# Kernel optimization log

Hardware: AMD Instinct MI355X
Metric: run time of the kernel (lower is better)

Reference implementation:

```python
import jax, jax.numpy as jnp
import numpy as np

B, S, D, H = 2, 2048, 2048, 16
DH = D // H  # 128
EPS = 1e-6


def _rms_norm(x, w):
    # RMSNorm over last dim with learnable scale
    var = jnp.mean(jnp.square(x), axis=-1, keepdims=True)
    return x * jax.lax.rsqrt(var + EPS) * w


def _apply_rope(x, angles):
    # x: [B, S, H, DH]; angles: [S, DH//2]; interleaved pair rotation
    xs = x.reshape(*x.shape[:-1], DH // 2, 2)
    x0, x1 = xs[..., 0], xs[..., 1]
    cos = jnp.cos(angles)[None, :, None, :]  # [1,S,1,DH/2]
    sin = jnp.sin(angles)[None, :, None, :]
    r0 = x0 * cos - x1 * sin
    r1 = x0 * sin + x1 * cos
    return jnp.stack([r0, r1], axis=-1).reshape(x.shape)


def setup_inputs() -> dict:
    key = jax.random.key(0)
    ks = jax.random.split(key, 4)
    x = jax.random.normal(ks[0], (B, S, D), dtype=jnp.float32)
    # standard RoPE angle table: pos * inv_freq
    inv_freq = 1.0 / (10000.0 ** (jnp.arange(0, DH, 2, dtype=jnp.float32) / DH))
    pos = jnp.arange(S, dtype=jnp.float32)
    rp_freqs = pos[:, None] * inv_freq[None, :]  # [S, DH/2]
    Win = jax.random.normal(ks[1], (3 * D, D), dtype=jnp.float32) * (D ** -0.5)
    b_in = jnp.zeros((3 * D,), dtype=jnp.float32)
    Wout = jax.random.normal(ks[2], (D, D), dtype=jnp.float32) * (D ** -0.5)
    b_out = jnp.zeros((D,), dtype=jnp.float32)
    qk_w = jnp.ones((DH,), dtype=jnp.float32)
    out_w = jnp.ones((D,), dtype=jnp.float32)
    return {"x": x, "rp_freqs": rp_freqs, "Win": Win, "b_in": b_in,
            "Wout": Wout, "b_out": b_out, "qk_w": qk_w, "out_w": out_w}


def reference(x, rp_freqs, Win, b_in, Wout, b_out, qk_w, out_w):
    b, s, d = x.shape
    qkv = jnp.einsum('bsd,ed->bse', x, Win) + b_in  # [B,S,3D]
    qkv = qkv.reshape(b, s, 3, H, DH)
    q, k, v = qkv[:, :, 0], qkv[:, :, 1], qkv[:, :, 2]  # each [B,S,H,DH]
    q = _apply_rope(q, rp_freqs)
    k = _apply_rope(k, rp_freqs)
    q = _rms_norm(q, qk_w)
    k = _rms_norm(k, qk_w)
    # causal SDPA, scale = 1/sqrt(DH) (default)
    a = jax.nn.dot_product_attention(q, k, v, is_causal=True)  # [B,S,H,DH]
    a = a.reshape(b, s, d)
    a = _rms_norm(a, out_w)
    return jnp.einsum('bsd,ed->bse', a, Wout) + b_out
```

## Files before the change

### kernel.cpp

```cpp
#include <hip/hip_runtime.h>
#include <cstdint>
#include <cstddef>

#define Bq  2
#define Sq  2048
#define Dq  2048
#define Hq  16
#define DHq 128
#define E3q 6144

typedef __attribute__((ext_vector_type(8))) short s16x8;
typedef __attribute__((ext_vector_type(4))) float f32x4;

__device__ __forceinline__ unsigned short f2bf(float f){
  union { float f; unsigned u; } v; v.f = f;
  unsigned r = v.u + 0x7FFFu + ((v.u >> 16) & 1u);
  return (unsigned short)(r >> 16);
}
__device__ __forceinline__ float bf2f(unsigned short b){
  union { unsigned u; float f; } v; v.u = ((unsigned)b) << 16;
  return v.f;
}
__device__ __forceinline__ unsigned cvtpk_bf16(float lo, float hi){
  unsigned r;
  asm("v_cvt_pk_bf16_f32 %0, %1, %2" : "=v"(r) : "v"(lo), "v"(hi));
  return r;
}

__device__ __forceinline__ void gload_lds16(const void* g, void* l){
  __builtin_amdgcn_global_load_lds(
      (const __attribute__((address_space(1))) void*)g,
      (__attribute__((address_space(3))) void*)l, 16, 0, 0);
}

__global__ __launch_bounds__(256) void k_convert3(const float* __restrict__ x,
                                                  const float* __restrict__ win,
                                                  const float* __restrict__ wout,
                                                  const float* __restrict__ out_w,
                                                  const float* __restrict__ rp,
                                                  unsigned short* __restrict__ xb,
                                                  unsigned short* __restrict__ wb,
                                                  unsigned short* __restrict__ woutb,
                                                  float2* __restrict__ rpcs){
  const int NX = (Bq*Sq*Dq)/4;
  const int NW = (E3q*Dq)/4;
  const int NO = (Dq*Dq)/4;
  const int NR = (Sq*64)/4;
  const int total = NX + NW + NO + NR;
  int stride = gridDim.x * blockDim.x;
  for (int i = blockIdx.x*blockDim.x + threadIdx.x; i < total; i += stride){
    if (i < NX + NW){
      const float* src; unsigned short* dst; int j;
      if (i < NX){ src = x; dst = xb; j = i; }
      else { src = win; dst = wb; j = i - NX; }
      float4 v = reinterpret_cast<const float4*>(src)[j];
      ushort4 o;
      o.x = f2bf(v.x); o.y = f2bf(v.y); o.z = f2bf(v.z); o.w = f2bf(v.w);
      reinterpret_cast<ushort4*>(dst)[j] = o;
    } else if (i < NX + NW + NO){
      int j = i - NX - NW;
      float4 v = reinterpret_cast<const float4*>(wout)[j];
      float4 w = reinterpret_cast<const float4*>(out_w)[j & 511];
      ushort4 o;
      o.x = f2bf(v.x*w.x); o.y = f2bf(v.y*w.y); o.z = f2bf(v.z*w.z); o.w = f2bf(v.w*w.w);
      reinterpret_cast<ushort4*>(woutb)[j] = o;
    } else {
      int j = i - NX - NW - NO;
      float4 a = reinterpret_cast<const float4*>(rp)[j];
      float sn0,cs0,sn1,cs1,sn2,cs2,sn3,cs3;
      sincosf(a.x,&sn0,&cs0); sincosf(a.y,&sn1,&cs1);
      sincosf(a.z,&sn2,&cs2); sincosf(a.w,&sn3,&cs3);
      float4 p0 = make_float4(cs0,sn0,cs1,sn1);
      float4 p1 = make_float4(cs2,sn2,cs3,sn3);
      reinterpret_cast<float4*>(rpcs)[j*2  ] = p0;
      reinterpret_cast<float4*>(rpcs)[j*2+1] = p1;
    }
  }
}

__global__ __launch_bounds__(512, 1) void k_gemm1f(const unsigned short* __restrict__ A,
                                                   const unsigned short* __restrict__ Bt,
                                                   const float* __restrict__ bias,
                                                   const float2* __restrict__ rpcs,
                                                   const float* __restrict__ qk_w,
                                                   unsigned short* __restrict__ Qp,
                                                   unsigned short* __restrict__ Kp,
                                                   unsigned short* __restrict__ Vt){
  const int K = 2048, NI = 16;
  const int bid = blockIdx.x;
  const int xcd = bid & 7, u = bid >> 3;
  const int m0 = (xcd*4 + (u & 3)) * 128;
  const int n0 = (u >> 2) * 256;

  const int tid = threadIdx.x;
  const int lane = tid & 63, w = tid >> 6, g = lane >> 4, c = lane & 15;
  const int wm = w >> 2, wn = w & 3;

  __shared__ __align__(16) unsigned short L[49152];

  const int srow = tid >> 2, spc = tid & 3;
  const int ssw = (spc ^ ((srow >> 1) & 3)) << 3;
  const unsigned short* aSrc  = A  + (size_t)(m0 + srow      )*K + ssw;
  const unsigned short* bSrc0 = Bt + (size_t)(n0 + srow      )*K + ssw;
  const unsigned short* bSrc1 = Bt + (size_t)(n0 + srow + 128)*K + ssw;

  auto stA = [&](int t, int h){
    gload_lds16(aSrc + t*64 + h*32, &L[((t&1)*2 + h)*4096 + tid*8]);
  };
  auto stB = [&](int t, int h, int uu){
    const unsigned short* s = (uu==0) ? bSrc0 : bSrc1;
    gload_lds16(s + t*64 + h*32, &L[16384 + ((t&1)*2 + h)*8192 + uu*4096 + tid*8]);
  };

  int aoff[4], boff[4];
#pragma unroll
  for (int mf=0; mf<4; ++mf){
    int row = wm*64 + mf*16 + c;
    aoff[mf] = row*32 + ((g ^ ((row>>1)&3)) << 3);
  }
#pragma unroll
  for (int nf=0; nf<4; ++nf){
    int row = wn*64 + nf*16 + c;
    boff[nf] = row*32 + ((g ^ ((row>>1)&3)) << 3);
  }

  f32x4 acc[4][4];
#pragma unroll
  for (int i=0;i<4;i++)
#pragma unroll
    for (int j=0;j<4;j++)
#pragma unroll
      for (int r=0;r<4;r++) acc[i][j][r] = 0.f;

  auto RDA = [&](int b, int h, s16x8* af){
    const int ab = (b*2 + h)*4096;
#pragma unroll
    for (int mf=0; mf<4; ++mf) af[mf] = *(const s16x8*)&L[ab + aoff[mf]];
  };
  auto RDB = [&](int b, int h, int nh, s16x8* bf){
    const int bb = 16384 + (b*2 + h)*8192;
#pragma unroll
    for (int j=0; j<2; ++j) bf[j] = *(const s16x8*)&L[bb + boff[nh*2 + j]];
  };
  auto MM = [&](s16x8* af, s16x8* bf, int nh){
    __builtin_amdgcn_s_setprio(1);
#pragma unroll
    for (int mf=0; mf<4; ++mf)
#pragma unroll
      for (int j=0; j<2; ++j)
        acc[mf][nh*2+j] = __builtin_amdgcn_mfma_f32_16x16x32_bf16(af[mf], bf[j], acc[mf][nh*2+j], 0,0,0);
    __builtin_amdgcn_s_setprio(0);
  };
  auto BAR = [&](){
    __builtin_amdgcn_sched_barrier(0);
    __builtin_amdgcn_s_barrier();
    __builtin_amdgcn_sched_barrier(0);
  };

  stA(0,0); stB(0,0,0); stB(0,0,1);
  stA(0,1); stB(0,1,0); stB(0,1,1);
  stA(1,0); stB(1,0,0); stB(1,0,1);
  asm volatile("s_waitcnt vmcnt(3)" ::: "memory");
  __builtin_amdgcn_s_barrier();

  for (int i=0; i<NI; ++i){
    const int T0 = 2*i, T1 = 2*i + 1;
    const bool st = (i < NI-1);
    s16x8 af[4], bf[2];
    RDA(0,0,af); RDB(0,0,0,bf);
    stA(T1,1); stB(T1,1,0);
    BAR(); MM(af,bf,0); BAR();
    RDB(0,0,1,bf);
    stB(T1,1,1);
    BAR(); MM(af,bf,1); BAR();
    RDA(0,1,af); RDB(0,1,0,bf);
    if (st){ stA(T0+2,0); stB(T0+2,0,0); }
    BAR(); MM(af,bf,0); BAR();
    RDB(0,1,1,bf);
    if (st){ stB(T0+2,0,1); }
    __builtin_amdgcn_sched_barrier(0);
    if (st) asm volatile("s_waitcnt vmcnt(3)" ::: "memory");
    else    asm volatile("s_waitcnt vmcnt(0)" ::: "memory");
    BAR(); MM(af,bf,1); BAR();
    RDA(1,0,af); RDB(1,0,0,bf);
    if (st){ stA(T0+2,1); stB(T0+2,1,0); }
    BAR(); MM(af,bf,0); BAR();
    RDB(1,0,1,bf);
    if (st){ stB(T0+2,1,1); }
    BAR(); MM(af,bf,1); BAR();
    RDA(1,1,af); RDB(1,1,0,bf);
    if (st){ stA(T1+2,0); stB(T1+2,0,0); }
    BAR(); MM(af,bf,0); BAR();
    RDB(1,1,1,bf);
    if (st){ stB(T1+2,0,1); }
    __builtin_amdgcn_sched_barrier(0);
    if (st) asm volatile("s_waitcnt vmcnt(3)" ::: "memory");
    else    asm volatile("s_waitcnt vmcnt(0)" ::: "memory");
    BAR(); MM(af,bf,1); BAR();
  }

  const int btype = (n0 < 2048) ? 0 : (n0 < 4096) ? 1 : 2;
  const int b  = m0 >> 11;
  const int sb = m0 & 2047;
  const int h0 = (n0 & 2047) >> 7;
  const int LTS = 264;
  const float QSCALE = 0.08838834764831845f * 1.4426950408889634f;

#pragma unroll
  for (int nf=0; nf<4; ++nf){
    const float bv = bias[n0 + wn*64 + nf*16 + c];
#pragma unroll
    for (int mf=0; mf<4; ++mf)
#pragma unroll
      for (int r=0; r<4; ++r) acc[mf][nf][r] += bv;
  }

  __syncthreads();

  if (btype < 2){
    float s2[4][4];
#pragma unroll
    for (int mf=0;mf<4;mf++)
#pragma unroll
      for (int r=0;r<4;r++){
        float s = 0.f;
#pragma unroll
        for (int nf=0;nf<4;nf++){ float v = acc[mf][nf][r]; s += v*v; }
        s2[mf][r] = s;
      }
#pragma unroll
    for (int m=1;m<16;m<<=1)
#pragma unroll
      for (int mf=0;mf<4;mf++)
#pragma unroll
        for (int r=0;r<4;r++) s2[mf][r] += __shfl_xor(s2[mf][r], m);
    float* Ssum = (float*)&L[0];
    if (c==0 && (wn&1)==0){
#pragma unroll
      for (int mf=0;mf<4;mf++)
#pragma unroll
        for (int r=0;r<4;r++)
          Ssum[(wm*64+mf*16+g*4+r)*2 + (wn>>1)] = s2[mf][r];
    }
    __syncthreads();
    if (c==0 && (wn&1)==1){
#pragma unroll
      for (int mf=0;mf<4;mf++)
#pragma unroll
        for (int r=0;r<4;r++)
          Ssum[(wm*64+mf*16+g*4+r)*2 + (wn>>1)] += s2[mf][r];
    }
    __syncthreads();
    float rsc[4][4];
#pragma unroll
    for (int mf=0;mf<4;mf++)
#pragma unroll
      for (int r=0;r<4;r++)
        rsc[mf][r] = rsqrtf(Ssum[(wm*64+mf*16+g*4+r)*2 + (wn>>1)]*(1.f/128.f) + 1e-6f);
    __syncthreads();

    const float qmul = (btype==0) ? QSCALE : 1.f;
    float wq[4];
    int pp[4];
#pragma unroll
    for (int nf=0;nf<4;nf++){
      wq[nf] = qk_w[(wn*64+nf*16+c)&127];
      pp[nf] = ((wn*64+nf*16+c)&127) >> 1;
    }

#pragma unroll
    for (int mf=0;mf<4;mf++)
#pragma unroll
      for (int r=0;r<4;r++){
        const int rowl = wm*64+mf*16+g*4+r;
        const int s = sb + rowl;
        const float sc = rsc[mf][r] * qmul;
#pragma unroll
        for (int nf=0;nf<4;nf++){
          float2 t = rpcs[s*64 + pp[nf]];
          float v  = acc[mf][nf][r];
          float pv = __shfl_xor(v, 1);
          float rot = ((c&1)==0) ? (v*t.x - pv*t.y) : (pv*t.y + v*t.x);
          L[rowl*LTS + wn*64+nf*16+c] = f2bf(rot * sc * wq[nf]);
        }
      }
    __syncthreads();
    {
      const int rw = tid >> 2, hd = (tid>>1)&1, hf = tid&1;
      const int bh = b*Hq + h0 + hd;
      unsigned short* dst = ((btype==0) ? Qp : Kp)
                          + ((size_t)bh*Sq + sb + rw)*DHq + hf*64;
      const unsigned short* srcl = &L[rw*LTS + hd*128 + hf*64];
#pragma unroll
      for (int i2=0;i2<8;i2++)
        *(s16x8*)&dst[i2*8] = *(const s16x8*)&srcl[i2*8];
    }
  } else {
#pragma unroll
    for (int mf=0;mf<4;mf++)
#pragma unroll
      for (int r=0;r<4;r++){
        const int rowl = wm*64+mf*16+g*4+r;
#pragma unroll
        for (int nf=0;nf<4;nf++)
          L[rowl*LTS + wn*64+nf*16+c] = f2bf(acc[mf][nf][r]);
      }
    __syncthreads();
    {
      const int dh2 = tid >> 1, hfr = (tid & 1) * 64;
      const int hd = dh2 >> 7, dh = dh2 & 127;
      const int bh = b*Hq + h0 + hd;
      unsigned short buf[64];
#pragma unroll
      for (int i2=0;i2<64;i2++) buf[i2] = L[(hfr+i2)*LTS + dh2];
      unsigned short* dst = Vt + ((size_t)bh*DHq + dh)*Sq + sb + hfr;
#pragma unroll
      for (int i2=0;i2<8;i2++)
        *(s16x8*)&dst[i2*8] = *(const s16x8*)&buf[i2*8];
    }
  }
}

__global__ __launch_bounds__(512, 1) void k_gemm2_8ph(const unsigned short* __restrict__ A,
                                                      const unsigned short* __restrict__ Bt,
                                                      const float* __restrict__ bias,
                                                      const float* __restrict__ ssqp,
                                                      float* __restrict__ C){
  const int K = 2048, N = 2048, NI = 16;
  const int bid = blockIdx.x;
  const int xcd = bid & 7, u = bid >> 3;
  const int m0 = (xcd*4 + (u & 3)) * 128;
  const int n0 = (u >> 2) * 256;

  const int tid = threadIdx.x;
  const int lane = tid & 63, w = tid >> 6, g = lane >> 4, c = lane & 15;
  const int wm = w >> 2, wn = w & 3;

  __shared__ __align__(16) unsigned short L[49152];

  const int srow = tid >> 2, spc = tid & 3;
  const int ssw = (spc ^ ((srow >> 1) & 3)) << 3;
  const unsigned short* aSrc  = A  + (size_t)(m0 + srow      )*K + ssw;
  const unsigned short* bSrc0 = Bt + (size_t)(n0 + srow      )*K + ssw;
  const unsigned short* bSrc1 = Bt + (size_t)(n0 + srow + 128)*K + ssw;

  auto stA = [&](int t, int h){
    gload_lds16(aSrc + t*64 + h*32, &L[((t&1)*2 + h)*4096 + tid*8]);
  };
  auto stB = [&](int t, int h, int uu){
    const unsigned short* s = (uu==0) ? bSrc0 : bSrc1;
    gload_lds16(s + t*64 + h*32, &L[16384 + ((t&1)*2 + h)*8192 + uu*4096 + tid*8]);
  };

  int aoff[4], boff[4];
#pragma unroll
  for (int mf=0; mf<4; ++mf){
    int row = wm*64 + mf*16 + c;
    aoff[mf] = row*32 + ((g ^ ((row>>1)&3)) << 3);
  }
#pragma unroll
  for (int nf=0; nf<4; ++nf){
    int row = wn*64 + nf*16 + c;
    boff[nf] = row*32 + ((g ^ ((row>>1)&3)) << 3);
  }

  f32x4 acc[4][4];
#pragma unroll
  for (int i=0;i<4;i++)
#pragma unroll
    for (int j=0;j<4;j++)
#pragma unroll
      for (int r=0;r<4;r++) acc[i][j][r] = 0.f;

  auto RDA = [&](int b, int h, s16x8* af){
    const int ab = (b*2 + h)*4096;
#pragma unroll
    for (int mf=0; mf<4; ++mf) af[mf] = *(const s16x8*)&L[ab + aoff[mf]];
  };
  auto RDB = [&](int b, int h, int nh, s16x8* bf){
    const int bb = 16384 + (b*2 + h)*8192;
#pragma unroll
    for (int j=0; j<2; ++j) bf[j] = *(const s16x8*)&L[bb + boff[nh*2 + j]];
  };
  auto MM = [&](s16x8* af, s16x8* bf, int nh){
    __builtin_amdgcn_s_setprio(1);
#pragma unroll
    for (int mf=0; mf<4; ++mf)
#pragma unroll
      for (int j=0; j<2; ++j)
        acc[mf][nh*2+j] = __builtin_amdgcn_mfma_f32_16x16x32_bf16(af[mf], bf[j], acc[mf][nh*2+j], 0,0,0);
    __builtin_amdgcn_s_setprio(0);
  };
  auto BAR = [&](){
    __builtin_amdgcn_sched_barrier(0);
    __builtin_amdgcn_s_barrier();
    __builtin_amdgcn_sched_barrier(0);
  };

  stA(0,0); stB(0,0,0); stB(0,0,1);
  stA(0,1); stB(0,1,0); stB(0,1,1);
  stA(1,0); stB(1,0,0); stB(1,0,1);
  asm volatile("s_waitcnt vmcnt(3)" ::: "memory");
  __builtin_amdgcn_s_barrier();

  for (int i=0; i<NI; ++i){
    const int T0 = 2*i, T1 = 2*i + 1;
    const bool st = (i < NI-1);
    s16x8 af[4], bf[2];
    RDA(0,0,af); RDB(0,0,0,bf);
    stA(T1,1); stB(T1,1,0);
    BAR(); MM(af,bf,0); BAR();
    RDB(0,0,1,bf);
    stB(T1,1,1);
    BAR(); MM(af,bf,1); BAR();
    RDA(0,1,af); RDB(0,1,0,bf);
    if (st){ stA(T0+2,0); stB(T0+2,0,0); }
    BAR(); MM(af,bf,0); BAR();
    RDB(0,1,1,bf);
    if (st){ stB(T0+2,0,1); }
    __builtin_amdgcn_sched_barrier(0);
    if (st) asm volatile("s_waitcnt vmcnt(3)" ::: "memory");
    else    asm volatile("s_waitcnt vmcnt(0)" ::: "memory");
    BAR(); MM(af,bf,1); BAR();
    RDA(1,0,af); RDB(1,0,0,bf);
    if (st){ stA(T0+2,1); stB(T0+2,1,0); }
    BAR(); MM(af,bf,0); BAR();
    RDB(1,0,1,bf);
    if (st){ stB(T0+2,1,1); }
    BAR(); MM(af,bf,1); BAR();
    RDA(1,1,af); RDB(1,1,0,bf);
    if (st){ stA(T1+2,0); stB(T1+2,0,0); }
    BAR(); MM(af,bf,0); BAR();
    RDB(1,1,1,bf);
    if (st){ stB(T1+2,0,1); }
    __builtin_amdgcn_sched_barrier(0);
    if (st) asm volatile("s_waitcnt vmcnt(3)" ::: "memory");
    else    asm volatile("s_waitcnt vmcnt(0)" ::: "memory");
    BAR(); MM(af,bf,1); BAR();
  }

  __syncthreads();
  float* SS = (float*)&L[0];
  if (tid < 128){
    const float* p = ssqp + (size_t)(m0 + tid)*16;
    float s = 0.f;
#pragma unroll
    for (int h=0; h<16; ++h) s += p[h];
    SS[tid] = rsqrtf(s*(1.f/2048.f) + 1e-6f);
  }
  __syncthreads();

#pragma unroll
  for (int nf=0; nf<4; ++nf){
    const int col = n0 + wn*64 + nf*16 + c;
    const float bv = bias[col];
#pragma unroll
    for (int mf=0; mf<4; ++mf){
      const int rowl = wm*64 + mf*16 + g*4;
#pragma unroll
      for (int r=0; r<4; ++r)
        C[(size_t)(m0+rowl+r)*N + col] = acc[mf][nf][r]*SS[rowl+r] + bv;
    }
  }
}

__global__ __launch_bounds__(256, 2) void k_attn(const unsigned short* __restrict__ Qp,
                                                 const unsigned short* __restrict__ Kp,
                                                 const unsigned short* __restrict__ Vt,
                                                 unsigned short* __restrict__ Ar,
                                                 float* __restrict__ ssqp){
  const int L = blockIdx.x;
  const int xcdL = L & 7, j = L >> 3;
  const int bh = xcdL*4 + ((j & 31) >> 3);
  const int qtile = (j < 32) ? (8 + (j & 7)) : (7 - (j & 7));
  const int b = bh >> 4, h = bh & 15;
  const int tid = threadIdx.x;
  const int w = tid >> 6, lane = tid & 63, g = lane >> 4, c = lane & 15;
  const int r0w = qtile*128 + w*32;

  const unsigned short* Qh = Qp + (size_t)bh * Sq * DHq;
  const unsigned short* Kh = Kp + (size_t)bh * Sq * DHq;
  const unsigned short* Vh = Vt + (size_t)bh * DHq * Sq;

  __shared__ __align__(16) unsigned short Ks[2][64*128];
  __shared__ __align__(16) unsigned short Vs[2][128*64];
  __shared__ __align__(16) unsigned short Pl[4][32*64];
  unsigned short* Pw = &Pl[w][0];

  s16x8 qf[2][4];
#pragma unroll
  for (int mi=0;mi<2;mi++)
#pragma unroll
    for (int kc=0;kc<4;kc++)
      qf[mi][kc] = *(const s16x8*)&Qh[(size_t)(r0w + mi*16 + c)*DHq + kc*32 + g*8];

  f32x4 acc[2][8];
#pragma unroll
  for (int mi=0;mi<2;mi++)
#pragma unroll
    for (int dt=0;dt<8;dt++)
#pragma unroll
      for (int r=0;r<4;r++) acc[mi][dt][r] = 0.f;
  float m_r[2] = { -INFINITY, -INFINITY };
  float l_p[2] = { 0.f, 0.f };

  const int nsteps = 2*qtile + 2;

  auto stage = [&](int j0s, int bufi){
#pragma unroll
    for (int i=0;i<4;i++){
      int pk = tid + i*256;
      int row = pk>>4, pcc = pk&15;
      gload_lds16(&Kh[(size_t)(j0s+row)*DHq + ((pcc^(row&7))<<3)], &Ks[bufi][pk*8]);
    }
#pragma unroll
    for (int i=0;i<4;i++){
      int pk = tid + i*256;
      int row = pk>>3, pcc = pk&7;
      gload_lds16(&Vh[(size_t)row*Sq + j0s + ((pcc^(row&7))<<3)], &Vs[bufi][pk*8]);
    }
  };

  stage(0, 0);
  __syncthreads();

  for (int t=0; t<nsteps; ++t){
    const int j0 = t*64;
    if (t+1 < nsteps) stage((t+1)*64, (t+1)&1);

    if (j0 <= r0w + 31){
      const unsigned short* Kc = &Ks[t&1][0];
      const unsigned short* Vc = &Vs[t&1][0];

      f32x4 sv[2][4];
#pragma unroll
      for (int mi=0;mi<2;mi++)
#pragma unroll
        for (int js=0;js<4;js++)
#pragma unroll
          for (int r=0;r<4;r++) sv[mi][js][r] = 0.f;

      __builtin_amdgcn_s_setprio(1);
#pragma unroll
      for (int js=0;js<4;js++){
        s16x8 kf[4];
#pragma unroll
        for (int kc=0;kc<4;kc++)
          kf[kc] = *(const s16x8*)&Kc[(js*16 + c)*128 + (((kc*4+g)^(c&7))<<3)];
#pragma unroll
        for (int mi=0;mi<2;mi++)
#pragma unroll
          for (int kc=0;kc<4;kc++)
            sv[mi][js] = __builtin_amdgcn_mfma_f32_16x16x32_bf16(kf[kc], qf[mi][kc], sv[mi][js], 0,0,0);
      }
      __builtin_amdgcn_s_setprio(0);

      if (j0 + 63 > r0w){
#pragma unroll
        for (int mi=0;mi<2;mi++){
          const int q = r0w + mi*16 + c;
#pragma unroll
          for (int js=0;js<4;js++)
#pragma unroll
            for (int r=0;r<4;r++)
              if (j0 + js*16 + g*4 + r > q) sv[mi][js][r] = -INFINITY;
        }
      }

      float pmx[2];
#pragma unroll
      for (int mi=0;mi<2;mi++){
        float mx = fmaxf(fmaxf(sv[mi][0][0],sv[mi][0][1]), fmaxf(sv[mi][0][2],sv[mi][0][3]));
#pragma unroll
        for (int js=1;js<4;js++){
          float a = fmaxf(fmaxf(sv[mi][js][0],sv[mi][js][1]), fmaxf(sv[mi][js][2],sv[mi][js][3]));
          mx = fmaxf(mx, a);
        }
        mx = fmaxf(mx, __shfl_xor(mx, 16));
        mx = fmaxf(mx, __shfl_xor(mx, 32));
        pmx[mi] = mx;
      }
      int need = (pmx[0] > m_r[0] + 8.f) | (pmx[1] > m_r[1] + 8.f);
      if (__any(need)){
#pragma unroll
        for (int mi=0;mi<2;mi++){
          float mnew = fmaxf(m_r[mi], pmx[mi]);
          float corr = exp2f(m_r[mi] - mnew);
          l_p[mi] *= corr;
          m_r[mi] = mnew;
#pragma unroll
          for (int dt=0;dt<8;dt++)
#pragma unroll
            for (int r=0;r<4;r++) acc[mi][dt][r] *= corr;
        }
      }
#pragma unroll
      for (int mi=0;mi<2;mi++){
        const float mm = m_r[mi];
        const int rowoff = (mi*16 + c)*64;
#pragma unroll
        for (int js=0;js<4;js++){
          float e0 = exp2f(sv[mi][js][0] - mm);
          float e1 = exp2f(sv[mi][js][1] - mm);
          float e2 = exp2f(sv[mi][js][2] - mm);
          float e3 = exp2f(sv[mi][js][3] - mm);
          l_p[mi] += (e0+e1)+(e2+e3);
          uint2 pk2;
          pk2.x = cvtpk_bf16(e0, e1);
          pk2.y = cvtpk_bf16(e2, e3);
          const int kc8 = js*2 + (g>>1);
          *(uint2*)&Pw[rowoff + ((kc8 ^ (c&7))<<3) + (g&1)*4] = pk2;
        }
      }

      s16x8 pfr[2][2];
#pragma unroll
      for (int mi=0;mi<2;mi++)
#pragma unroll
        for (int kc=0;kc<2;kc++)
          pfr[mi][kc] = *(const s16x8*)&Pw[(mi*16 + c)*64 + (((kc*4+g)^(c&7))<<3)];
      __builtin_amdgcn_s_setprio(1);
#pragma unroll
      for (int dt=0; dt<8; dt++){
#pragma unroll
        for (int kc=0;kc<2;kc++){
          s16x8 vfr = *(const s16x8*)&Vc[(dt*16 + c)*64 + (((kc*4+g)^(c&7))<<3)];
#pragma unroll
          for (int mi=0;mi<2;mi++)
            acc[mi][dt] = __builtin_amdgcn_mfma_f32_16x16x32_bf16(vfr, pfr[mi][kc], acc[mi][dt], 0,0,0);
        }
      }
      __builtin_amdgcn_s_setprio(0);
    }
    __syncthreads();
  }

#pragma unroll
  for (int mi=0;mi<2;mi++){
    float l = l_p[mi];
    l += __shfl_xor(l, 16);
    l += __shfl_xor(l, 32);
    const float inv = 1.f / l;
    const int row = r0w + mi*16 + c;
    unsigned short* dst = &Ar[((size_t)(b*Sq + row))*Dq + h*DHq];
    float sq = 0.f;
#pragma unroll
    for (int dt=0; dt<8; dt++){
      float v0 = acc[mi][dt][0]*inv, v1 = acc[mi][dt][1]*inv;
      float v2 = acc[mi][dt][2]*inv, v3 = acc[mi][dt][3]*inv;
      sq += v0*v0 + v1*v1 + v2*v2 + v3*v3;
      uint2 o2;
      o2.x = cvtpk_bf16(v0, v1);
      o2.y = cvtpk_bf16(v2, v3);
      *(uint2*)&dst[dt*16 + g*4] = o2;
    }
    sq += __shfl_xor(sq, 16);
    sq += __shfl_xor(sq, 32);
    if (g == 0)
      ssqp[(size_t)(b*Sq + row)*16 + h] = sq;
  }
}

extern "C" void kernel_launch(void* const* d_in, const int* in_sizes, int n_in,
                              void* d_out, int out_size, void* d_ws, size_t ws_size,
                              hipStream_t stream){
  const float* x     = (const float*)d_in[0];
  const float* rp    = (const float*)d_in[1];
  const float* Win   = (const float*)d_in[2];
  const float* b_in  = (const float*)d_in[3];
  const float* Wout  = (const float*)d_in[4];
  const float* b_out = (const float*)d_in[5];
  const float* qk_w  = (const float*)d_in[6];
  const float* out_w = (const float*)d_in[7];
  float* outp = (float*)d_out;

  if (ws_size < (160ull<<20)) return;

  char* ws = (char*)d_ws;
  unsigned short* Xb    = (unsigned short*)(ws);
  unsigned short* Wb    = (unsigned short*)(ws + (16ull<<20));
  unsigned short* Woutb = (unsigned short*)(ws + (40ull<<20));
  float*          ssqp  = (float*)         (ws + (48ull<<20));
  float2*         rpcs  = (float2*)        (ws + (49ull<<20));
  unsigned short* Qp    = (unsigned short*)(ws + (96ull<<20));
  unsigned short* Kp    = (unsigned short*)(ws + (112ull<<20));
  unsigned short* Vt    = (unsigned short*)(ws + (128ull<<20));
  unsigned short* Ar    = (unsigned short*)(ws + (144ull<<20));

  k_convert3<<<2048, 256, 0, stream>>>(x, Win, Wout, out_w, rp, Xb, Wb, Woutb, rpcs);
  k_gemm1f<<<768, 512, 0, stream>>>(Xb, Wb, b_in, rpcs, qk_w, Qp, Kp, Vt);
  k_attn<<<512, 256, 0, stream>>>(Qp, Kp, Vt, Ar, ssqp);
  k_gemm2_8ph<<<256, 512, 0, stream>>>(Ar, Woutb, b_out, ssqp, outp);
}
```

Before: 262.0 us.

## Widen QKV GEMM tile to 128x384 so 512 blocks cover the grid once

The fused QKV projection kernel now computes 128x384 output tiles instead of 128x256, so the grid shrinks from 768 to 512 blocks. With one block per CU, that should avoid a partial second wave on the 256-CU device and raise A-tile reuse. A 384-wide tile can straddle head and Q/K/V boundaries, so the epilogue now tracks two heads per wave for the RMS sums and writes per column type. LDS use grows to 128KB and the accumulator registers grow by half, which may pressure occupancy and registers.

```diff
diff --git a/kernel.cpp b/kernel.cpp
--- a/kernel.cpp
+++ b/kernel.cpp
@@ -86,7 +86,275 @@
                                                    unsigned short* __restrict__ Qp,
                                                    unsigned short* __restrict__ Kp,
                                                    unsigned short* __restrict__ Vt){
-  const int K = 2048, NI = 16;
+  const int K = 2048;
+  const int bid = blockIdx.x;
+  const int xcd = bid & 7, u = bid >> 3;
+  const int m0 = (xcd*4 + (u & 3)) * 128;
+  const int n0 = (u >> 2) * 384;
+
+  const int tid = threadIdx.x;
+  const int lane = tid & 63, w = tid >> 6, g = lane >> 4, c = lane & 15;
+  const int wm = w >> 2, wn = w & 3;
+
+  __shared__ __align__(16) unsigned short L[65536];
+
+  const int srow = tid >> 2, spc = tid & 3;
+  const int ssw = (spc ^ ((srow >> 1) & 3)) << 3;
+  const unsigned short* aSrc  = A  + (size_t)(m0 + srow      )*K + ssw;
+  const unsigned short* bSrc0 = Bt + (size_t)(n0 + srow      )*K + ssw;
+  const unsigned short* bSrc1 = Bt + (size_t)(n0 + srow + 128)*K + ssw;
+  const unsigned short* bSrc2 = Bt + (size_t)(n0 + srow + 256)*K + ssw;
+
+  auto stA = [&](int t, int h){
+    gload_lds16(aSrc + t*64 + h*32, &L[((t&1)*2 + h)*4096 + tid*8]);
+  };
+  auto stB = [&](int t, int h, int uu){
+    const unsigned short* s = (uu==0) ? bSrc0 : (uu==1) ? bSrc1 : bSrc2;
+    gload_lds16(s + t*64 + h*32, &L[16384 + ((t&1)*2 + h)*12288 + uu*4096 + tid*8]);
+  };
+
+  int aoff[4], boff[6];
+#pragma unroll
+  for (int mf=0; mf<4; ++mf){
+    int row = wm*64 + mf*16 + c;
+    aoff[mf] = row*32 + ((g ^ ((row>>1)&3)) << 3);
+  }
+#pragma unroll
+  for (int nf=0; nf<6; ++nf){
+    int row = wn*96 + nf*16 + c;
+    boff[nf] = row*32 + ((g ^ ((row>>1)&3)) << 3);
+  }
+
+  f32x4 acc[4][6];
+#pragma unroll
+  for (int i=0;i<4;i++)
+#pragma unroll
+    for (int j=0;j<6;j++)
+#pragma unroll
+      for (int r=0;r<4;r++) acc[i][j][r] = 0.f;
+
+  auto RDA = [&](int b, int h, s16x8* af){
+    const int ab = (b*2 + h)*4096;
+#pragma unroll
+    for (int mf=0; mf<4; ++mf) af[mf] = *(const s16x8*)&L[ab + aoff[mf]];
+  };
+  auto RDB = [&](int b, int h, int nh, s16x8* bf){
+    const int bb = 16384 + (b*2 + h)*12288;
+#pragma unroll
+    for (int j=0; j<3; ++j) bf[j] = *(const s16x8*)&L[bb + boff[nh*3 + j]];
+  };
+  auto MM = [&](s16x8* af, s16x8* bf, int nh){
+    __builtin_amdgcn_s_setprio(1);
+#pragma unroll
+    for (int mf=0; mf<4; ++mf)
+#pragma unroll
+      for (int j=0; j<3; ++j)
+        acc[mf][nh*3+j] = __builtin_amdgcn_mfma_f32_16x16x32_bf16(af[mf], bf[j], acc[mf][nh*3+j], 0,0,0);
+    __builtin_amdgcn_s_setprio(0);
+  };
+  auto BAR = [&](){
+    __builtin_amdgcn_sched_barrier(0);
+    __builtin_amdgcn_s_barrier();
+    __builtin_amdgcn_sched_barrier(0);
+  };
+
+  stA(0,0); stB(0,0,0); stB(0,0,1); stB(0,0,2);
+  stA(0,1); stB(0,1,0); stB(0,1,1); stB(0,1,2);
+  stA(1,0); stB(1,0,0); stB(1,0,1); stB(1,0,2);
+  asm volatile("s_waitcnt vmcnt(4)" ::: "memory");
+  __builtin_amdgcn_s_barrier();
+
+  for (int i=0; i<16; ++i){
+    const int T0 = 2*i, T1 = 2*i + 1;
+    const bool st = (i < 15);
+    s16x8 af[4], bf[3];
+    RDA(0,0,af); RDB(0,0,0,bf);
+    stA(T1,1); stB(T1,1,0);
+    BAR(); MM(af,bf,0); BAR();
+    RDB(0,0,1,bf);
+    stB(T1,1,1); stB(T1,1,2);
+    BAR(); MM(af,bf,1); BAR();
+    RDA(0,1,af); RDB(0,1,0,bf);
+    if (st){ stA(T0+2,0); stB(T0+2,0,0); }
+    BAR(); MM(af,bf,0); BAR();
+    RDB(0,1,1,bf);
+    if (st){ stB(T0+2,0,1); stB(T0+2,0,2); }
+    __builtin_amdgcn_sched_barrier(0);
+    if (st) asm volatile("s_waitcnt vmcnt(4)" ::: "memory");
+    else    asm volatile("s_waitcnt vmcnt(0)" ::: "memory");
+    BAR(); MM(af,bf,1); BAR();
+    RDA(1,0,af); RDB(1,0,0,bf);
+    if (st){ stA(T0+2,1); stB(T0+2,1,0); }
+    BAR(); MM(af,bf,0); BAR();
+    RDB(1,0,1,bf);
+    if (st){ stB(T0+2,1,1); stB(T0+2,1,2); }
+    BAR(); MM(af,bf,1); BAR();
+    RDA(1,1,af); RDB(1,1,0,bf);
+    if (st){ stA(T1+2,0); stB(T1+2,0,0); }
+    BAR(); MM(af,bf,0); BAR();
+    RDB(1,1,1,bf);
+    if (st){ stB(T1+2,0,1); stB(T1+2,0,2); }
+    __builtin_amdgcn_sched_barrier(0);
+    if (st) asm volatile("s_waitcnt vmcnt(4)" ::: "memory");
+    else    asm volatile("s_waitcnt vmcnt(0)" ::: "memory");
+    BAR(); MM(af,bf,1); BAR();
+  }
+
+  const int b  = m0 >> 11;
+  const int sb = m0 & 2047;
+  const int LTS = 392;
+  const float QSCALE = 0.08838834764831845f * 1.4426950408889634f;
+  const int hdA = (wn*96) >> 7;
+
+#pragma unroll
+  for (int nf=0; nf<6; ++nf){
+    const float bv = bias[n0 + wn*96 + nf*16 + c];
+#pragma unroll
+    for (int mf=0; mf<4; ++mf)
+#pragma unroll
+      for (int r=0; r<4; ++r) acc[mf][nf][r] += bv;
+  }
+
+  __syncthreads();
+
+  float sA[4][4], sB[4][4];
+#pragma unroll
+  for (int mf=0;mf<4;mf++)
+#pragma unroll
+    for (int r=0;r<4;r++){ sA[mf][r] = 0.f; sB[mf][r] = 0.f; }
+#pragma unroll
+  for (int nf=0; nf<6; ++nf){
+    const int hd_nf = (wn*96 + nf*16) >> 7;
+    if (hd_nf == hdA){
+#pragma unroll
+      for (int mf=0;mf<4;mf++)
+#pragma unroll
+        for (int r=0;r<4;r++){ float v = acc[mf][nf][r]; sA[mf][r] += v*v; }
+    } else {
+#pragma unroll
+      for (int mf=0;mf<4;mf++)
+#pragma unroll
+        for (int r=0;r<4;r++){ float v = acc[mf][nf][r]; sB[mf][r] += v*v; }
+    }
+  }
+#pragma unroll
+  for (int m=1;m<16;m<<=1)
+#pragma unroll
+    for (int mf=0;mf<4;mf++)
+#pragma unroll
+      for (int r=0;r<4;r++){
+        sA[mf][r] += __shfl_xor(sA[mf][r], m);
+        sB[mf][r] += __shfl_xor(sB[mf][r], m);
+      }
+
+  float* SS = (float*)&L[50176];
+  if (c == 0){
+#pragma unroll
+    for (int mf=0;mf<4;mf++)
+#pragma unroll
+      for (int r=0;r<4;r++){
+        const int row = wm*64 + mf*16 + g*4 + r;
+        if (wn == 0) SS[row*3 + 0] = sA[mf][r];
+        else if (wn == 1) SS[row*3 + 1] = sB[mf][r];
+        else if (wn == 2) SS[row*3 + 2] = sB[mf][r];
+      }
+  }
+  __syncthreads();
+  if (c == 0){
+#pragma unroll
+    for (int mf=0;mf<4;mf++)
+#pragma unroll
+      for (int r=0;r<4;r++){
+        const int row = wm*64 + mf*16 + g*4 + r;
+        if (wn == 1) SS[row*3 + 0] += sA[mf][r];
+        else if (wn == 2) SS[row*3 + 1] += sA[mf][r];
+        else if (wn == 3) SS[row*3 + 2] += sA[mf][r];
+      }
+  }
+  __syncthreads();
+
+  const int hdB = (hdA < 2) ? hdA + 1 : 2;
+  float rA[4][4], rB[4][4];
+#pragma unroll
+  for (int mf=0;mf<4;mf++)
+#pragma unroll
+    for (int r=0;r<4;r++){
+      const int row = wm*64 + mf*16 + g*4 + r;
+      rA[mf][r] = rsqrtf(SS[row*3 + hdA]*(1.f/128.f) + 1e-6f);
+      rB[mf][r] = rsqrtf(SS[row*3 + hdB]*(1.f/128.f) + 1e-6f);
+    }
+  __syncthreads();
+
+  float wq[6]; int pp[6];
+#pragma unroll
+  for (int nf=0;nf<6;nf++){
+    const int cw = (wn*96 + nf*16 + c) & 127;
+    wq[nf] = qk_w[cw];
+    pp[nf] = cw >> 1;
+  }
+#pragma unroll
+  for (int nf=0; nf<6; ++nf){
+    const int colw = wn*96 + nf*16 + c;
+    const int bt = (n0 + colw) >> 11;
+    const int hd_nf = colw >> 7;
+    if (bt < 2){
+#pragma unroll
+      for (int mf=0;mf<4;mf++)
+#pragma unroll
+        for (int r=0;r<4;r++){
+          const int row = wm*64 + mf*16 + g*4 + r;
+          const float rs = (hd_nf == hdA) ? rA[mf][r] : rB[mf][r];
+          const float sc = rs * ((bt==0) ? QSCALE : 1.f);
+          float v  = acc[mf][nf][r];
+          float pv = __shfl_xor(v, 1);
+          float2 t = rpcs[(sb + row)*64 + pp[nf]];
+          float rot = ((c&1)==0) ? (v*t.x - pv*t.y) : (pv*t.y + v*t.x);
+          L[row*LTS + colw] = f2bf(rot * sc * wq[nf]);
+        }
+    } else {
+#pragma unroll
+      for (int mf=0;mf<4;mf++)
+#pragma unroll
+        for (int r=0;r<4;r++){
+          const int row = wm*64 + mf*16 + g*4 + r;
+          L[row*LTS + colw] = f2bf(acc[mf][nf][r]);
+        }
+    }
+  }
+  __syncthreads();
+
+#pragma unroll
+  for (int hd=0; hd<3; ++hd){
+    const int base = n0 + hd*128;
+    if (base < 4096){
+      const bool isQ = (base < 2048);
+      const int bh = b*Hq + ((base & 2047) >> 7);
+      const int rw = tid >> 2, part = tid & 3;
+      unsigned short* dst = (isQ ? Qp : Kp) + ((size_t)bh*Sq + sb + rw)*DHq + part*32;
+      const unsigned short* srcl = &L[rw*LTS + hd*128 + part*32];
+#pragma unroll
+      for (int i2=0;i2<4;i2++)
+        *(s16x8*)&dst[i2*8] = *(const s16x8*)&srcl[i2*8];
+    } else {
+      const int bh = b*Hq + ((base - 4096) >> 7);
+      const int dh = tid & 127, sg = tid >> 7;
+      unsigned short buf[32];
+#pragma unroll
+      for (int i2=0;i2<32;i2++) buf[i2] = L[(sg*32 + i2)*LTS + hd*128 + dh];
+      unsigned short* dst = Vt + ((size_t)bh*DHq + dh)*Sq + sb + sg*32;
+#pragma unroll
+      for (int i2=0;i2<4;i2++)
+        *(s16x8*)&dst[i2*8] = *(const s16x8*)&buf[i2*8];
+    }
+  }
+}
+
+__global__ __launch_bounds__(512, 1) void k_gemm2_8ph(const unsigned short* __restrict__ A,
+                                                      const unsigned short* __restrict__ Bt,
+                                                      const float* __restrict__ bias,
+                                                      const float* __restrict__ ssqp,
+                                                      float* __restrict__ C){
+  const int K = 2048, N = 2048, NI = 16;
   const int bid = blockIdx.x;
   const int xcd = bid & 7, u = bid >> 3;
   const int m0 = (xcd*4 + (u & 3)) * 128;
@@ -199,246 +467,6 @@
     BAR(); MM(af,bf,1); BAR();
   }
 
-  const int btype = (n0 < 2048) ? 0 : (n0 < 4096) ? 1 : 2;
-  const int b  = m0 >> 11;
-  const int sb = m0 & 2047;
-  const int h0 = (n0 & 2047) >> 7;
-  const int LTS = 264;
-  const float QSCALE = 0.08838834764831845f * 1.4426950408889634f;
-
-#pragma unroll
-  for (int nf=0; nf<4; ++nf){
-    const float bv = bias[n0 + wn*64 + nf*16 + c];
-#pragma unroll
-    for (int mf=0; mf<4; ++mf)
-#pragma unroll
-      for (int r=0; r<4; ++r) acc[mf][nf][r] += bv;
-  }
-
-  __syncthreads();
-
-  if (btype < 2){
-    float s2[4][4];
-#pragma unroll
-    for (int mf=0;mf<4;mf++)
-#pragma unroll
-      for (int r=0;r<4;r++){
-        float s = 0.f;
-#pragma unroll
-        for (int nf=0;nf<4;nf++){ float v = acc[mf][nf][r]; s += v*v; }
-        s2[mf][r] = s;
-      }
-#pragma unroll
-    for (int m=1;m<16;m<<=1)
-#pragma unroll
-      for (int mf=0;mf<4;mf++)
-#pragma unroll
-        for (int r=0;r<4;r++) s2[mf][r] += __shfl_xor(s2[mf][r], m);
-    float* Ssum = (float*)&L[0];
-    if (c==0 && (wn&1)==0){
-#pragma unroll
-      for (int mf=0;mf<4;mf++)
-#pragma unroll
-        for (int r=0;r<4;r++)
-          Ssum[(wm*64+mf*16+g*4+r)*2 + (wn>>1)] = s2[mf][r];
-    }
-    __syncthreads();
-    if (c==0 && (wn&1)==1){
-#pragma unroll
-      for (int mf=0;mf<4;mf++)
-#pragma unroll
-        for (int r=0;r<4;r++)
-          Ssum[(wm*64+mf*16+g*4+r)*2 + (wn>>1)] += s2[mf][r];
-    }
-    __syncthreads();
-    float rsc[4][4];
-#pragma unroll
-    for (int mf=0;mf<4;mf++)
-#pragma unroll
-      for (int r=0;r<4;r++)
-        rsc[mf][r] = rsqrtf(Ssum[(wm*64+mf*16+g*4+r)*2 + (wn>>1)]*(1.f/128.f) + 1e-6f);
-    __syncthreads();
-
-    const float qmul = (btype==0) ? QSCALE : 1.f;
-    float wq[4];
-    int pp[4];
-#pragma unroll
-    for (int nf=0;nf<4;nf++){
-      wq[nf] = qk_w[(wn*64+nf*16+c)&127];
-      pp[nf] = ((wn*64+nf*16+c)&127) >> 1;
-    }
-
-#pragma unroll
-    for (int mf=0;mf<4;mf++)
-#pragma unroll
-      for (int r=0;r<4;r++){
-        const int rowl = wm*64+mf*16+g*4+r;
-        const int s = sb + rowl;
-        const float sc = rsc[mf][r] * qmul;
-#pragma unroll
-        for (int nf=0;nf<4;nf++){
-          float2 t = rpcs[s*64 + pp[nf]];
-          float v  = acc[mf][nf][r];
-          float pv = __shfl_xor(v, 1);
-          float rot = ((c&1)==0) ? (v*t.x - pv*t.y) : (pv*t.y + v*t.x);
-          L[rowl*LTS + wn*64+nf*16+c] = f2bf(rot * sc * wq[nf]);
-        }
-      }
-    __syncthreads();
-    {
-      const int rw = tid >> 2, hd = (tid>>1)&1, hf = tid&1;
-      const int bh = b*Hq + h0 + hd;
-      unsigned short* dst = ((btype==0) ? Qp : Kp)
-                          + ((size_t)bh*Sq + sb + rw)*DHq + hf*64;
-      const unsigned short* srcl = &L[rw*LTS + hd*128 + hf*64];
-#pragma unroll
-      for (int i2=0;i2<8;i2++)
-        *(s16x8*)&dst[i2*8] = *(const s16x8*)&srcl[i2*8];
-    }
-  } else {
-#pragma unroll
-    for (int mf=0;mf<4;mf++)
-#pragma unroll
-      for (int r=0;r<4;r++){
-        const int rowl = wm*64+mf*16+g*4+r;
-#pragma unroll
-        for (int nf=0;nf<4;nf++)
-          L[rowl*LTS + wn*64+nf*16+c] = f2bf(acc[mf][nf][r]);
-      }
-    __syncthreads();
-    {
-      const int dh2 = tid >> 1, hfr = (tid & 1) * 64;
-      const int hd = dh2 >> 7, dh = dh2 & 127;
-      const int bh = b*Hq + h0 + hd;
-      unsigned short buf[64];
-#pragma unroll
-      for (int i2=0;i2<64;i2++) buf[i2] = L[(hfr+i2)*LTS + dh2];
-      unsigned short* dst = Vt + ((size_t)bh*DHq + dh)*Sq + sb + hfr;
-#pragma unroll
-      for (int i2=0;i2<8;i2++)
-        *(s16x8*)&dst[i2*8] = *(const s16x8*)&buf[i2*8];
-    }
-  }
-}
-
-__global__ __launch_bounds__(512, 1) void k_gemm2_8ph(const unsigned short* __restrict__ A,
-                                                      const unsigned short* __restrict__ Bt,
-                                                      const float* __restrict__ bias,
-                                                      const float* __restrict__ ssqp,
-                                                      float* __restrict__ C){
-  const int K = 2048, N = 2048, NI = 16;
-  const int bid = blockIdx.x;
-  const int xcd = bid & 7, u = bid >> 3;
-  const int m0 = (xcd*4 + (u & 3)) * 128;
-  const int n0 = (u >> 2) * 256;
-
-  const int tid = threadIdx.x;
-  const int lane = tid & 63, w = tid >> 6, g = lane >> 4, c = lane & 15;
-  const int wm = w >> 2, wn = w & 3;
-
-  __shared__ __align__(16) unsigned short L[49152];
-
-  const int srow = tid >> 2, spc = tid & 3;
-  const int ssw = (spc ^ ((srow >> 1) & 3)) << 3;
-  const unsigned short* aSrc  = A  + (size_t)(m0 + srow      )*K + ssw;
-  const unsigned short* bSrc0 = Bt + (size_t)(n0 + srow      )*K + ssw;
-  const unsigned short* bSrc1 = Bt + (size_t)(n0 + srow + 128)*K + ssw;
-
-  auto stA = [&](int t, int h){
-    gload_lds16(aSrc + t*64 + h*32, &L[((t&1)*2 + h)*4096 + tid*8]);
-  };
-  auto stB = [&](int t, int h, int uu){
-    const unsigned short* s = (uu==0) ? bSrc0 : bSrc1;
-    gload_lds16(s + t*64 + h*32, &L[16384 + ((t&1)*2 + h)*8192 + uu*4096 + tid*8]);
-  };
-
-  int aoff[4], boff[4];
-#pragma unroll
-  for (int mf=0; mf<4; ++mf){
-    int row = wm*64 + mf*16 + c;
-    aoff[mf] = row*32 + ((g ^ ((row>>1)&3)) << 3);
-  }
-#pragma unroll
-  for (int nf=0; nf<4; ++nf){
-    int row = wn*64 + nf*16 + c;
-    boff[nf] = row*32 + ((g ^ ((row>>1)&3)) << 3);
-  }
-
-  f32x4 acc[4][4];
-#pragma unroll
-  for (int i=0;i<4;i++)
-#pragma unroll
-    for (int j=0;j<4;j++)
-#pragma unroll
-      for (int r=0;r<4;r++) acc[i][j][r] = 0.f;
-
-  auto RDA = [&](int b, int h, s16x8* af){
-    const int ab = (b*2 + h)*4096;
-#pragma unroll
-    for (int mf=0; mf<4; ++mf) af[mf] = *(const s16x8*)&L[ab + aoff[mf]];
-  };
-  auto RDB = [&](int b, int h, int nh, s16x8* bf){
-    const int bb = 16384 + (b*2 + h)*8192;
-#pragma unroll
-    for (int j=0; j<2; ++j) bf[j] = *(const s16x8*)&L[bb + boff[nh*2 + j]];
-  };
-  auto MM = [&](s16x8* af, s16x8* bf, int nh){
-    __builtin_amdgcn_s_setprio(1);
-#pragma unroll
-    for (int mf=0; mf<4; ++mf)
-#pragma unroll
-      for (int j=0; j<2; ++j)
-        acc[mf][nh*2+j] = __builtin_amdgcn_mfma_f32_16x16x32_bf16(af[mf], bf[j], acc[mf][nh*2+j], 0,0,0);
-    __builtin_amdgcn_s_setprio(0);
-  };
-  auto BAR = [&](){
-    __builtin_amdgcn_sched_barrier(0);
-    __builtin_amdgcn_s_barrier();
-    __builtin_amdgcn_sched_barrier(0);
-  };
-
-  stA(0,0); stB(0,0,0); stB(0,0,1);
-  stA(0,1); stB(0,1,0); stB(0,1,1);
-  stA(1,0); stB(1,0,0); stB(1,0,1);
-  asm volatile("s_waitcnt vmcnt(3)" ::: "memory");
-  __builtin_amdgcn_s_barrier();
-
-  for (int i=0; i<NI; ++i){
-    const int T0 = 2*i, T1 = 2*i + 1;
-    const bool st = (i < NI-1);
-    s16x8 af[4], bf[2];
-    RDA(0,0,af); RDB(0,0,0,bf);
-    stA(T1,1); stB(T1,1,0);
-    BAR(); MM(af,bf,0); BAR();
-    RDB(0,0,1,bf);
-    stB(T1,1,1);
-    BAR(); MM(af,bf,1); BAR();
-    RDA(0,1,af); RDB(0,1,0,bf);
-    if (st){ stA(T0+2,0); stB(T0+2,0,0); }
-    BAR(); MM(af,bf,0); BAR();
-    RDB(0,1,1,bf);
-    if (st){ stB(T0+2,0,1); }
-    __builtin_amdgcn_sched_barrier(0);
-    if (st) asm volatile("s_waitcnt vmcnt(3)" ::: "memory");
-    else    asm volatile("s_waitcnt vmcnt(0)" ::: "memory");
-    BAR(); MM(af,bf,1); BAR();
-    RDA(1,0,af); RDB(1,0,0,bf);
-    if (st){ stA(T0+2,1); stB(T0+2,1,0); }
-    BAR(); MM(af,bf,0); BAR();
-    RDB(1,0,1,bf);
-    if (st){ stB(T0+2,1,1); }
-    BAR(); MM(af,bf,1); BAR();
-    RDA(1,1,af); RDB(1,1,0,bf);
-    if (st){ stA(T1+2,0); stB(T1+2,0,0); }
-    BAR(); MM(af,bf,0); BAR();
-    RDB(1,1,1,bf);
-    if (st){ stB(T1+2,0,1); }
-    __builtin_amdgcn_sched_barrier(0);
-    if (st) asm volatile("s_waitcnt vmcnt(3)" ::: "memory");
-    else    asm volatile("s_waitcnt vmcnt(0)" ::: "memory");
-    BAR(); MM(af,bf,1); BAR();
-  }
-
   __syncthreads();
   float* SS = (float*)&L[0];
   if (tid < 128){
@@ -688,7 +716,7 @@
   unsigned short* Ar    = (unsigned short*)(ws + (144ull<<20));
 
   k_convert3<<<2048, 256, 0, stream>>>(x, Win, Wout, out_w, rp, Xb, Wb, Woutb, rpcs);
-  k_gemm1f<<<768, 512, 0, stream>>>(Xb, Wb, b_in, rpcs, qk_w, Qp, Kp, Vt);
+  k_gemm1f<<<512, 512, 0, stream>>>(Xb, Wb, b_in, rpcs, qk_w, Qp, Kp, Vt);
   k_attn<<<512, 256, 0, stream>>>(Qp, Kp, Vt, Ar, ssqp);
   k_gemm2_8ph<<<256, 512, 0, stream>>>(Ar, Woutb, b_out, ssqp, outp);
 }
```

After: 273.3 us. 1.04x slower.
